# Performance work log

Hardware: AMD Instinct MI355X
Metric: run time of the kernel (lower is better)

Reference implementation:

```python
import jax, jax.numpy as jnp
import numpy as np

B, IN, H, OUT, RANK = 2048, 256, 128, 128, 8
EPS = 1e-5

def setup_inputs() -> dict:
    key = jax.random.key(0)
    ks = jax.random.split(key, 9)
    inv = lambda n: 1.0 / np.sqrt(n)
    return {
        "X": jax.random.normal(ks[0], (B, IN), jnp.float32),
        "W1": jax.random.uniform(ks[1], (IN, H), jnp.float32, -inv(IN), inv(IN)),
        "b1": jnp.zeros((H,), jnp.float32),
        "W2": jax.random.uniform(ks[2], (IN, OUT), jnp.float32, -inv(IN), inv(IN)),
        "b2": jnp.zeros((OUT,), jnp.float32),
        "W3": jax.random.uniform(ks[3], (H, OUT), jnp.float32, -inv(H), inv(H)),
        "b3": jnp.zeros((OUT,), jnp.float32),
        "P": jax.random.normal(ks[4], (RANK, H, H, H), jnp.float32),  # (rank, p, q, k)
        "gz": jnp.ones((H,), jnp.float32),
        "bz": jnp.zeros((H,), jnp.float32),
        "gy": jnp.ones((H,), jnp.float32),
        "by": jnp.zeros((H,), jnp.float32),
    }

def _bn(x, g, b):
    # training-mode BatchNorm1d: batch stats, biased variance
    m = x.mean(axis=0)
    v = x.var(axis=0)
    return (x - m) * jax.lax.rsqrt(v + EPS) * g + b

def reference(X, W1, b1, W2, b2, W3, b3, P, gz, bz, gy, by):
    Z = jax.nn.relu(X @ W1 + b1)               # (B, H); dropout = identity (eval)

    def step(carry, Pi):
        Zi, Y = carry
        # batch_quadratic: out[b,k] = sum_{p,q} Zi[b,p] * Pi[p,q,k] * Z[b,q]
        Zi = jnp.einsum('bp,pqk,bq->bk', Zi, Pi, Z)
        Zi = _bn(Zi, gz, bz)
        return (Zi, Y + Zi / RANK), None

    Y0 = jnp.zeros((X.shape[0], H), X.dtype)
    (_, Y), _ = jax.lax.scan(step, (Z, Y0), P)
    Y = _bn(Y, gy, by)
    out = jax.nn.relu(jax.nn.relu(Y @ W3 + b3) + jax.nn.relu(X @ W2 + b2))
    return out
```

## Files before the change

### kernel.cpp

```cpp
#include <hip/hip_runtime.h>

typedef __bf16 bf16x8 __attribute__((ext_vector_type(8)));
typedef float  floatx4 __attribute__((ext_vector_type(4)));

constexpr int B_    = 2048;
constexpr int NIN   = 256;
constexpr int H_    = 128;
constexpr int RANK_ = 8;
constexpr float EPS_ = 1e-5f;

__global__ __launch_bounds__(256)
void k_head(const float* __restrict__ X,
            const float* __restrict__ W1, const float* __restrict__ b1,
            const float* __restrict__ W2, const float* __restrict__ b2,
            const float* __restrict__ P,
            float* __restrict__ R2, __bf16* __restrict__ Zbf,
            __bf16* __restrict__ Pperm, float* __restrict__ stats ) {
    __shared__ float smem[4160];
    const int bx = blockIdx.x, t = threadIdx.x;

    if (bx < RANK_ + 1) stats[bx * 256 + t] = 0.f;

    if (bx < 512) {
        const int b0 = bx * 4;
#pragma unroll
        for (int i = 0; i < 4; ++i) {
            const int e = i * 256 + t;
            smem[e] = X[(size_t)(b0 + (e >> 8)) * NIN + (e & 255)];
        }
        __syncthreads();
        const int col = t & 127, rh = t >> 7;
        float s1a = 0.f, s2a = 0.f, s1b = 0.f, s2b = 0.f;
        const float* sxa = smem + rh * 256;
        const float* sxb = smem + (rh + 2) * 256;
#pragma unroll 8
        for (int i = 0; i < NIN; ++i) {
            const float w1 = W1[i * H_ + col];
            const float w2 = W2[i * H_ + col];
            s1a = fmaf(sxa[i], w1, s1a);  s2a = fmaf(sxa[i], w2, s2a);
            s1b = fmaf(sxb[i], w1, s1b);  s2b = fmaf(sxb[i], w2, s2b);
        }
        const int ba = b0 + rh, bb = b0 + rh + 2;
        const float za = fmaxf(s1a + b1[col], 0.f), ra = fmaxf(s2a + b2[col], 0.f);
        const float zb = fmaxf(s1b + b1[col], 0.f), rb = fmaxf(s2b + b2[col], 0.f);
        Zbf[(size_t)ba * H_ + col] = (__bf16)za;  R2[(size_t)ba * H_ + col] = ra;
        Zbf[(size_t)bb * H_ + col] = (__bf16)zb;  R2[(size_t)bb * H_ + col] = rb;
        __syncthreads();
    }
    {
        const int r = bx >> 7, p = bx & 127;
        const float4* Pp4 = (const float4*)(P + ((size_t)r * H_ + p) * (H_ * H_));
        __bf16* dst = Pperm + (size_t)r * (H_ * H_ * H_);
        const int L = t & 63, quad = L >> 4, lo = L & 15, g0 = t >> 6;

        float4 rg[4][4];
#pragma unroll
        for (int s = 0; s < 4; ++s)
#pragma unroll
            for (int it = 0; it < 4; ++it) {
                const int idx = it * 256 + t;
                rg[s][it] = Pp4[(size_t)(s * 32 + (idx >> 5)) * 32 + (idx & 31)];
            }
#pragma unroll
        for (int s = 0; s < 4; ++s) {
            if (s) __syncthreads();
#pragma unroll
            for (int it = 0; it < 4; ++it) {
                const int idx = it * 256 + t;
                float* d = smem + (idx >> 5) * 129 + (idx & 31) * 4;
                d[0] = rg[s][it].x; d[1] = rg[s][it].y;
                d[2] = rg[s][it].z; d[3] = rg[s][it].w;
            }
            __syncthreads();
#pragma unroll
            for (int gg = 0; gg < 2; ++gg) {
                const int g = g0 + 4 * gg;
                __bf16 v8[8];
#pragma unroll
                for (int j = 0; j < 8; ++j)
                    v8[j] = (__bf16)smem[(quad * 8 + j) * 129 + g * 16 + lo];
                *(bf16x8*)(dst + (((size_t)(g * 128 + p) * 4 + s) * 64 + L) * 8) =
                    *(const bf16x8*)v8;
            }
        }
    }
}

__global__ __launch_bounds__(512, 2)
void k_rank(const __bf16* __restrict__ Pr, const __bf16* __restrict__ Zbf,
            const float* __restrict__ prevT, const float* __restrict__ prevStats,
            const float* __restrict__ gz, const float* __restrict__ bz,
            float* __restrict__ T, float* __restrict__ stats, const int first) {
    __shared__ float smem[8960];
    const int kg = blockIdx.x, mblk = blockIdx.y, b0 = mblk * 64;
    const int t = threadIdx.x;
    const int w = t >> 6, L = t & 63, quad = L >> 4, lo = L & 15;

    float* sAl = smem + 8704; float* sBe = smem + 8832;
    if (!first && t < 128) {
        const float s1 = prevStats[t], s2 = prevStats[128 + t];
        const float mm = s1 * (1.f / B_);
        const float var = s2 * (1.f / B_) - mm * mm;
        const float a = rsqrtf(var + EPS_) * gz[t];
        sAl[t] = a; sBe[t] = bz[t] - mm * a;
    }
    bf16x8 A[4][4];
#pragma unroll
    for (int mt = 0; mt < 4; ++mt)
#pragma unroll
        for (int ks = 0; ks < 4; ++ks)
            A[mt][ks] = *(const bf16x8*)(Zbf + (size_t)(b0 + mt * 16 + lo) * H_ + ks * 32 + quad * 8);

    const bf16x8* Pb = (const bf16x8*)Pr;
    const int p0 = w * 16;
    const size_t fbase = ((size_t)kg * 128 + p0) * 4;

#define LOADB(dst, pl) do {                                                   \
    _Pragma("unroll") for (int s_ = 0; s_ < 4; ++s_)                          \
        dst[s_] = Pb[(fbase + (size_t)(pl) * 4 + s_) * 64 + L];               \
} while (0)

    bf16x8 B0[4], B1[4], B2[4], B3[4];
    LOADB(B0, 0);
    LOADB(B1, 1);
    LOADB(B2, 2);
    LOADB(B3, 3);

    __syncthreads();
    {
        const int sp = t & 127, rr = t >> 7;
        if (first) {
#pragma unroll
            for (int i = 0; i < 16; ++i) {
                const int row = rr + 4 * i;
                smem[sp * 68 + row] = (float)Zbf[(size_t)(b0 + row) * H_ + sp];
            }
        } else {
            const float a = sAl[sp], be = sBe[sp];
#pragma unroll
            for (int i = 0; i < 16; ++i) {
                const int row = rr + 4 * i;
                smem[sp * 68 + row] = fmaf(prevT[(size_t)(b0 + row) * H_ + sp], a, be);
            }
        }
    }
    __syncthreads();

    floatx4 acc[4];
#pragma unroll
    for (int mt = 0; mt < 4; ++mt) acc[mt] = (floatx4){0.f, 0.f, 0.f, 0.f};

#define COMPUTE(Bx, pg) do {                                                  \
    floatx4 S_[4];                                                            \
    __builtin_amdgcn_s_setprio(1);                                            \
    _Pragma("unroll") for (int mt_ = 0; mt_ < 4; ++mt_)                       \
        S_[mt_] = __builtin_amdgcn_mfma_f32_16x16x32_bf16(                    \
            A[mt_][0], Bx[0], (floatx4){0.f, 0.f, 0.f, 0.f}, 0, 0, 0);        \
    _Pragma("unroll") for (int ks_ = 1; ks_ < 4; ++ks_)                       \
        _Pragma("unroll") for (int mt_ = 0; mt_ < 4; ++mt_)                   \
            S_[mt_] = __builtin_amdgcn_mfma_f32_16x16x32_bf16(                \
                A[mt_][ks_], Bx[ks_], S_[mt_], 0, 0, 0);                      \
    __builtin_amdgcn_s_setprio(0);                                            \
    _Pragma("unroll") for (int mt_ = 0; mt_ < 4; ++mt_) {                     \
        const floatx4 zi_ =                                                   \
            *(const floatx4*)&smem[(pg) * 68 + mt_ * 16 + quad * 4];          \
        acc[mt_] += zi_ * S_[mt_];                                            \
    }                                                                         \
} while (0)

#pragma unroll
    for (int pp = 0; pp < 16; pp += 4) {
        COMPUTE(B0, p0 + pp);     if (pp < 12) LOADB(B0, pp + 4);
        COMPUTE(B1, p0 + pp + 1); if (pp < 12) LOADB(B1, pp + 5);
        COMPUTE(B2, p0 + pp + 2); if (pp < 12) LOADB(B2, pp + 6);
        COMPUTE(B3, p0 + pp + 3); if (pp < 12) LOADB(B3, pp + 7);
    }
#undef LOADB
#undef COMPUTE

    __syncthreads();
#pragma unroll
    for (int mt = 0; mt < 4; ++mt)
#pragma unroll
        for (int i = 0; i < 4; ++i)
            smem[w * 1024 + (mt * 4 + i) * 64 + L] = acc[mt][i];
    if (t < 32) smem[8192 + t] = 0.f;
    __syncthreads();

    float cs = 0.f, cs2 = 0.f;
#pragma unroll
    for (int k2 = 0; k2 < 2; ++k2) {
        const int e = t + 512 * k2;
        float v = 0.f;
#pragma unroll
        for (int q = 0; q < 8; ++q) v += smem[q * 1024 + e];
        const int j = e >> 6, L2 = e & 63;
        const int row = b0 + (j >> 2) * 16 + (L2 >> 4) * 4 + (j & 3);
        const int col = kg * 16 + (L2 & 15);
        T[(size_t)row * H_ + col] = v;
        cs += v; cs2 += v * v;
    }
    cs  += __shfl_xor(cs, 16);  cs  += __shfl_xor(cs, 32);
    cs2 += __shfl_xor(cs2, 16); cs2 += __shfl_xor(cs2, 32);
    if (L < 16) { atomicAdd(&smem[8192 + L], cs); atomicAdd(&smem[8208 + L], cs2); }
    __syncthreads();
    if (t < 16)      atomicAdd(&stats[kg * 16 + t],            smem[8192 + t]);
    else if (t < 32) atomicAdd(&stats[128 + kg * 16 + t - 16], smem[8192 + t]);
}

__global__ __launch_bounds__(256)
void k_y(const float* __restrict__ T, const float* __restrict__ sums,
         const float* __restrict__ gz, const float* __restrict__ bz,
         float* __restrict__ Y, float* __restrict__ ysums) {
    __shared__ float al[1024], be[1024], red[256];
    const int bx = blockIdx.x, t = threadIdx.x;
    for (int e = t; e < 1024; e += 256) {
        const int rr = e >> 7, k = e & 127;
        const float s1 = sums[rr * 256 + k], s2 = sums[rr * 256 + 128 + k];
        const float mm = s1 * (1.f / B_);
        const float var = s2 * (1.f / B_) - mm * mm;
        const float a = rsqrtf(var + EPS_) * gz[k];
        al[e] = a; be[e] = bz[k] - mm * a;
    }
    red[t] = 0.f;
    __syncthreads();
    const int col = t & 127, half = t >> 7;
    float ps = 0.f, ps2 = 0.f;
    for (int i = 0; i < 16; ++i) {
        const int b = bx * 32 + half + 2 * i;
        float y = 0.f;
#pragma unroll
        for (int rr = 0; rr < 8; ++rr)
            y += fmaf(T[(size_t)rr * B_ * H_ + (size_t)b * H_ + col],
                      al[rr * 128 + col], be[rr * 128 + col]);
        y *= (1.f / RANK_);
        Y[(size_t)b * H_ + col] = y;
        ps += y; ps2 += y * y;
    }
    atomicAdd(&red[col],       half == 0 ? ps  : 0.f);
    atomicAdd(&red[128 + col], half == 0 ? ps2 : 0.f);
    __syncthreads();
    atomicAdd(&red[col],       half == 1 ? ps  : 0.f);
    atomicAdd(&red[128 + col], half == 1 ? ps2 : 0.f);
    __syncthreads();
    if (t < 128) {
        atomicAdd(&ysums[t],       red[t]);
        atomicAdd(&ysums[128 + t], red[128 + t]);
    }
}

__global__ __launch_bounds__(256)
void k_out(const float* __restrict__ Y, const float* __restrict__ ystats,
           const float* __restrict__ gy, const float* __restrict__ by,
           const float* __restrict__ W3, const float* __restrict__ b3,
           const float* __restrict__ R2, float* __restrict__ out) {
    __shared__ float sy[8 * 132];
    const int bx = blockIdx.x, t = threadIdx.x;
    const int col = t & 127, rh = t >> 7;
    const int b0 = bx * 8;
    const float mm = ystats[col] * (1.f / B_);
    const float var = ystats[128 + col] * (1.f / B_) - mm * mm;
    const float ay = rsqrtf(var + EPS_) * gy[col];
    const float bb = by[col] - mm * ay;
#pragma unroll
    for (int i = 0; i < 4; ++i) {
        const int row = rh + 2 * i;
        sy[row * 132 + col] = fmaf(Y[(size_t)(b0 + row) * H_ + col], ay, bb);
    }
    __syncthreads();
#pragma unroll
    for (int j = 0; j < 4; ++j) {
        const int row = rh * 4 + j;
        float s = 0.f;
        const float* syr = sy + row * 132;
#pragma unroll 8
        for (int h = 0; h < H_; ++h)
            s = fmaf(syr[h], W3[h * H_ + col], s);
        const size_t gi = (size_t)(b0 + row) * H_ + col;
        out[gi] = fmaxf(fmaxf(s + b3[col], 0.f) + R2[gi], 0.f);
    }
}

extern "C" void kernel_launch(void* const* d_in, const int* in_sizes, int n_in,
                              void* d_out, int out_size, void* d_ws, size_t ws_size,
                              hipStream_t stream) {
    const float* X  = (const float*)d_in[0];
    const float* W1 = (const float*)d_in[1];
    const float* b1 = (const float*)d_in[2];
    const float* W2 = (const float*)d_in[3];
    const float* b2 = (const float*)d_in[4];
    const float* W3 = (const float*)d_in[5];
    const float* b3 = (const float*)d_in[6];
    const float* P  = (const float*)d_in[7];
    const float* gz = (const float*)d_in[8];
    const float* bz = (const float*)d_in[9];
    const float* gy = (const float*)d_in[10];
    const float* by = (const float*)d_in[11];
    float* out = (float*)d_out;

    const size_t rankElems = (size_t)H_ * H_ * H_;

    char* wsb = (char*)d_ws;
    float* R2     = (float*)wsb;   wsb += (size_t)B_ * H_ * 4;
    float* Y      = (float*)wsb;   wsb += (size_t)B_ * H_ * 4;
    float* stats  = (float*)wsb;   wsb += (size_t)(RANK_ + 1) * 256 * 4;
    float* T      = (float*)wsb;   wsb += (size_t)RANK_ * B_ * H_ * 4;
    __bf16* Zbf   = (__bf16*)wsb;  wsb += (size_t)B_ * H_ * 2;
    __bf16* Pperm = (__bf16*)wsb;

    float* ysums = stats + RANK_ * 256;

    k_head<<<1024, 256, 0, stream>>>(X, W1, b1, W2, b2, P, R2, Zbf, Pperm, stats);

    for (int r = 0; r < RANK_; ++r) {
        const float* prevT = (r == 0) ? (const float*)Zbf : (T + (size_t)(r - 1) * B_ * H_);
        const float* prevS = (r == 0) ? stats : (stats + (r - 1) * 256);
        k_rank<<<dim3(8, 32), 512, 0, stream>>>(Pperm + (size_t)r * rankElems, Zbf,
                                                prevT, prevS, gz, bz,
                                                T + (size_t)r * B_ * H_, stats + r * 256,
                                                r == 0 ? 1 : 0);
    }

    k_y<<<64, 256, 0, stream>>>(T, stats, gz, bz, Y, ysums);
    k_out<<<256, 256, 0, stream>>>(Y, ysums, gy, by, W3, b3, R2, out);
}
```

Before: 275.2 us.

## Halve batch tile in rank kernel and head GEMM to raise block count

The rank kernel now handles 32 batch rows per block instead of 64, launching 512 blocks instead of 256, with half the A fragments, accumulators, shared memory and a two-deep instead of four-deep B prefetch, and launch bounds raised to allow 4 blocks per CU. The head kernel computes 2 rows per block across all 1024 blocks instead of 4 rows in the first 512. The aim is better occupancy and CU coverage on the small grid. The cost is that each block re-reads the full P slice for half as many rows, doubling P traffic per rank step, and the shallower prefetch hides less load latency.

```diff
diff --git a/kernel.cpp b/kernel.cpp
--- a/kernel.cpp
+++ b/kernel.cpp
@@ -21,30 +21,26 @@
 
     if (bx < RANK_ + 1) stats[bx * 256 + t] = 0.f;
 
-    if (bx < 512) {
-        const int b0 = bx * 4;
-#pragma unroll
-        for (int i = 0; i < 4; ++i) {
+    {
+        const int b0 = bx * 2;
+#pragma unroll
+        for (int i = 0; i < 2; ++i) {
             const int e = i * 256 + t;
             smem[e] = X[(size_t)(b0 + (e >> 8)) * NIN + (e & 255)];
         }
         __syncthreads();
         const int col = t & 127, rh = t >> 7;
-        float s1a = 0.f, s2a = 0.f, s1b = 0.f, s2b = 0.f;
-        const float* sxa = smem + rh * 256;
-        const float* sxb = smem + (rh + 2) * 256;
-#pragma unroll 8
+        float s1 = 0.f, s2 = 0.f;
+        const float* sx = smem + rh * 256;
+#pragma unroll 16
         for (int i = 0; i < NIN; ++i) {
             const float w1 = W1[i * H_ + col];
             const float w2 = W2[i * H_ + col];
-            s1a = fmaf(sxa[i], w1, s1a);  s2a = fmaf(sxa[i], w2, s2a);
-            s1b = fmaf(sxb[i], w1, s1b);  s2b = fmaf(sxb[i], w2, s2b);
+            s1 = fmaf(sx[i], w1, s1);  s2 = fmaf(sx[i], w2, s2);
         }
-        const int ba = b0 + rh, bb = b0 + rh + 2;
-        const float za = fmaxf(s1a + b1[col], 0.f), ra = fmaxf(s2a + b2[col], 0.f);
-        const float zb = fmaxf(s1b + b1[col], 0.f), rb = fmaxf(s2b + b2[col], 0.f);
-        Zbf[(size_t)ba * H_ + col] = (__bf16)za;  R2[(size_t)ba * H_ + col] = ra;
-        Zbf[(size_t)bb * H_ + col] = (__bf16)zb;  R2[(size_t)bb * H_ + col] = rb;
+        const int br = b0 + rh;
+        const float z = fmaxf(s1 + b1[col], 0.f), r = fmaxf(s2 + b2[col], 0.f);
+        Zbf[(size_t)br * H_ + col] = (__bf16)z;  R2[(size_t)br * H_ + col] = r;
         __syncthreads();
     }
     {
@@ -86,17 +82,17 @@
     }
 }
 
-__global__ __launch_bounds__(512, 2)
+__global__ __launch_bounds__(512, 4)
 void k_rank(const __bf16* __restrict__ Pr, const __bf16* __restrict__ Zbf,
             const float* __restrict__ prevT, const float* __restrict__ prevStats,
             const float* __restrict__ gz, const float* __restrict__ bz,
             float* __restrict__ T, float* __restrict__ stats, const int first) {
-    __shared__ float smem[8960];
-    const int kg = blockIdx.x, mblk = blockIdx.y, b0 = mblk * 64;
+    __shared__ float smem[4864];
+    const int kg = blockIdx.x, mblk = blockIdx.y, b0 = mblk * 32;
     const int t = threadIdx.x;
     const int w = t >> 6, L = t & 63, quad = L >> 4, lo = L & 15;
 
-    float* sAl = smem + 8704; float* sBe = smem + 8832;
+    float* sAl = smem + 4608; float* sBe = smem + 4736;
     if (!first && t < 128) {
         const float s1 = prevStats[t], s2 = prevStats[128 + t];
         const float mm = s1 * (1.f / B_);
@@ -104,9 +100,9 @@
         const float a = rsqrtf(var + EPS_) * gz[t];
         sAl[t] = a; sBe[t] = bz[t] - mm * a;
     }
-    bf16x8 A[4][4];
-#pragma unroll
-    for (int mt = 0; mt < 4; ++mt)
+    bf16x8 A[2][4];
+#pragma unroll
+    for (int mt = 0; mt < 2; ++mt)
 #pragma unroll
         for (int ks = 0; ks < 4; ++ks)
             A[mt][ks] = *(const bf16x8*)(Zbf + (size_t)(b0 + mt * 16 + lo) * H_ + ks * 32 + quad * 8);
@@ -120,92 +116,83 @@
         dst[s_] = Pb[(fbase + (size_t)(pl) * 4 + s_) * 64 + L];               \
 } while (0)
 
-    bf16x8 B0[4], B1[4], B2[4], B3[4];
+    bf16x8 B0[4], B1[4];
     LOADB(B0, 0);
     LOADB(B1, 1);
-    LOADB(B2, 2);
-    LOADB(B3, 3);
 
     __syncthreads();
     {
         const int sp = t & 127, rr = t >> 7;
         if (first) {
 #pragma unroll
-            for (int i = 0; i < 16; ++i) {
+            for (int i = 0; i < 8; ++i) {
                 const int row = rr + 4 * i;
-                smem[sp * 68 + row] = (float)Zbf[(size_t)(b0 + row) * H_ + sp];
+                smem[sp * 36 + row] = (float)Zbf[(size_t)(b0 + row) * H_ + sp];
             }
         } else {
             const float a = sAl[sp], be = sBe[sp];
 #pragma unroll
-            for (int i = 0; i < 16; ++i) {
+            for (int i = 0; i < 8; ++i) {
                 const int row = rr + 4 * i;
-                smem[sp * 68 + row] = fmaf(prevT[(size_t)(b0 + row) * H_ + sp], a, be);
+                smem[sp * 36 + row] = fmaf(prevT[(size_t)(b0 + row) * H_ + sp], a, be);
             }
         }
     }
     __syncthreads();
 
-    floatx4 acc[4];
-#pragma unroll
-    for (int mt = 0; mt < 4; ++mt) acc[mt] = (floatx4){0.f, 0.f, 0.f, 0.f};
+    floatx4 acc[2];
+#pragma unroll
+    for (int mt = 0; mt < 2; ++mt) acc[mt] = (floatx4){0.f, 0.f, 0.f, 0.f};
 
 #define COMPUTE(Bx, pg) do {                                                  \
-    floatx4 S_[4];                                                            \
+    floatx4 S_[2];                                                            \
     __builtin_amdgcn_s_setprio(1);                                            \
-    _Pragma("unroll") for (int mt_ = 0; mt_ < 4; ++mt_)                       \
+    _Pragma("unroll") for (int mt_ = 0; mt_ < 2; ++mt_)                       \
         S_[mt_] = __builtin_amdgcn_mfma_f32_16x16x32_bf16(                    \
             A[mt_][0], Bx[0], (floatx4){0.f, 0.f, 0.f, 0.f}, 0, 0, 0);        \
     _Pragma("unroll") for (int ks_ = 1; ks_ < 4; ++ks_)                       \
-        _Pragma("unroll") for (int mt_ = 0; mt_ < 4; ++mt_)                   \
+        _Pragma("unroll") for (int mt_ = 0; mt_ < 2; ++mt_)                   \
             S_[mt_] = __builtin_amdgcn_mfma_f32_16x16x32_bf16(                \
                 A[mt_][ks_], Bx[ks_], S_[mt_], 0, 0, 0);                      \
     __builtin_amdgcn_s_setprio(0);                                            \
-    _Pragma("unroll") for (int mt_ = 0; mt_ < 4; ++mt_) {                     \
+    _Pragma("unroll") for (int mt_ = 0; mt_ < 2; ++mt_) {                     \
         const floatx4 zi_ =                                                   \
-            *(const floatx4*)&smem[(pg) * 68 + mt_ * 16 + quad * 4];          \
+            *(const floatx4*)&smem[(pg) * 36 + mt_ * 16 + quad * 4];          \
         acc[mt_] += zi_ * S_[mt_];                                            \
     }                                                                         \
 } while (0)
 
 #pragma unroll
-    for (int pp = 0; pp < 16; pp += 4) {
-        COMPUTE(B0, p0 + pp);     if (pp < 12) LOADB(B0, pp + 4);
-        COMPUTE(B1, p0 + pp + 1); if (pp < 12) LOADB(B1, pp + 5);
-        COMPUTE(B2, p0 + pp + 2); if (pp < 12) LOADB(B2, pp + 6);
-        COMPUTE(B3, p0 + pp + 3); if (pp < 12) LOADB(B3, pp + 7);
+    for (int pp = 0; pp < 16; pp += 2) {
+        COMPUTE(B0, p0 + pp);     if (pp < 14) LOADB(B0, pp + 2);
+        COMPUTE(B1, p0 + pp + 1); if (pp < 14) LOADB(B1, pp + 3);
     }
 #undef LOADB
 #undef COMPUTE
 
     __syncthreads();
 #pragma unroll
-    for (int mt = 0; mt < 4; ++mt)
+    for (int mt = 0; mt < 2; ++mt)
 #pragma unroll
         for (int i = 0; i < 4; ++i)
-            smem[w * 1024 + (mt * 4 + i) * 64 + L] = acc[mt][i];
-    if (t < 32) smem[8192 + t] = 0.f;
-    __syncthreads();
-
-    float cs = 0.f, cs2 = 0.f;
-#pragma unroll
-    for (int k2 = 0; k2 < 2; ++k2) {
-        const int e = t + 512 * k2;
-        float v = 0.f;
-#pragma unroll
-        for (int q = 0; q < 8; ++q) v += smem[q * 1024 + e];
-        const int j = e >> 6, L2 = e & 63;
-        const int row = b0 + (j >> 2) * 16 + (L2 >> 4) * 4 + (j & 3);
-        const int col = kg * 16 + (L2 & 15);
-        T[(size_t)row * H_ + col] = v;
-        cs += v; cs2 += v * v;
-    }
+            smem[w * 512 + (mt * 4 + i) * 64 + L] = acc[mt][i];
+    if (t < 32) smem[4096 + t] = 0.f;
+    __syncthreads();
+
+    float v = 0.f;
+#pragma unroll
+    for (int q = 0; q < 8; ++q) v += smem[q * 512 + t];
+    const int j = t >> 6, L2 = t & 63;
+    const int row = b0 + (j >> 2) * 16 + (L2 >> 4) * 4 + (j & 3);
+    const int col = kg * 16 + (L2 & 15);
+    T[(size_t)row * H_ + col] = v;
+    float cs = v, cs2 = v * v;
     cs  += __shfl_xor(cs, 16);  cs  += __shfl_xor(cs, 32);
     cs2 += __shfl_xor(cs2, 16); cs2 += __shfl_xor(cs2, 32);
-    if (L < 16) { atomicAdd(&smem[8192 + L], cs); atomicAdd(&smem[8208 + L], cs2); }
-    __syncthreads();
-    if (t < 16)      atomicAdd(&stats[kg * 16 + t],            smem[8192 + t]);
-    else if (t < 32) atomicAdd(&stats[128 + kg * 16 + t - 16], smem[8192 + t]);
+    if (L < 16) { atomicAdd(&smem[4096 + L], cs); atomicAdd(&smem[4112 + L], cs2); }
+    __syncthreads();
+    if (t < 16)      atomicAdd(&stats[kg * 16 + t],            smem[4096 + t]);
+    else if (t < 32) atomicAdd(&stats[128 + kg * 16 + t - 16], smem[4096 + t]);
 }
 
 __global__ __launch_bounds__(256)
@@ -315,7 +302,7 @@
     for (int r = 0; r < RANK_; ++r) {
         const float* prevT = (r == 0) ? (const float*)Zbf : (T + (size_t)(r - 1) * B_ * H_);
         const float* prevS = (r == 0) ? stats : (stats + (r - 1) * 256);
-        k_rank<<<dim3(8, 32), 512, 0, stream>>>(Pperm + (size_t)r * rankElems, Zbf,
+        k_rank<<<dim3(8, 64), 512, 0, stream>>>(Pperm + (size_t)r * rankElems, Zbf,
                                                 prevT, prevS, gz, bz,
                                                 T + (size_t)r * B_ * H_, stats + r * 256,
                                                 r == 0 ? 1 : 0);
```

After: 283.9 us. +3.1%, slower.

## Fuse per-rank launches into one cooperative kernel with grid sync

Applied to the files above, without the earlier changes.

Replaces the eight separate k_rank launches with a single cooperative k_ranks kernel that loops over ranks and uses grid.sync between them, removing per-launch overhead and ramp-up/tail gaps. The head kernel also now spreads the X@W1/X@W2 work across all 1024 blocks (2 rows each) instead of 512 blocks with 4 rows. Cooperative launch needs all 256 blocks to be co-resident and adds grid-barrier cost. The head change trades per-thread reuse of weight loads for better balance.

```diff
diff --git a/kernel.cpp b/kernel.cpp
--- a/kernel.cpp
+++ b/kernel.cpp
@@ -1,4 +1,7 @@
 #include <hip/hip_runtime.h>
+#include <hip/hip_cooperative_groups.h>
+
+namespace cg = cooperative_groups;
 
 typedef __bf16 bf16x8 __attribute__((ext_vector_type(8)));
 typedef float  floatx4 __attribute__((ext_vector_type(4)));
@@ -21,30 +24,26 @@
 
     if (bx < RANK_ + 1) stats[bx * 256 + t] = 0.f;
 
-    if (bx < 512) {
-        const int b0 = bx * 4;
-#pragma unroll
-        for (int i = 0; i < 4; ++i) {
+    {
+        const int b0 = bx * 2;
+#pragma unroll
+        for (int i = 0; i < 2; ++i) {
             const int e = i * 256 + t;
             smem[e] = X[(size_t)(b0 + (e >> 8)) * NIN + (e & 255)];
         }
         __syncthreads();
         const int col = t & 127, rh = t >> 7;
-        float s1a = 0.f, s2a = 0.f, s1b = 0.f, s2b = 0.f;
-        const float* sxa = smem + rh * 256;
-        const float* sxb = smem + (rh + 2) * 256;
-#pragma unroll 8
+        float s1 = 0.f, s2 = 0.f;
+        const float* sx = smem + rh * 256;
+#pragma unroll 16
         for (int i = 0; i < NIN; ++i) {
             const float w1 = W1[i * H_ + col];
             const float w2 = W2[i * H_ + col];
-            s1a = fmaf(sxa[i], w1, s1a);  s2a = fmaf(sxa[i], w2, s2a);
-            s1b = fmaf(sxb[i], w1, s1b);  s2b = fmaf(sxb[i], w2, s2b);
-        }
-        const int ba = b0 + rh, bb = b0 + rh + 2;
-        const float za = fmaxf(s1a + b1[col], 0.f), ra = fmaxf(s2a + b2[col], 0.f);
-        const float zb = fmaxf(s1b + b1[col], 0.f), rb = fmaxf(s2b + b2[col], 0.f);
-        Zbf[(size_t)ba * H_ + col] = (__bf16)za;  R2[(size_t)ba * H_ + col] = ra;
-        Zbf[(size_t)bb * H_ + col] = (__bf16)zb;  R2[(size_t)bb * H_ + col] = rb;
+            s1 = fmaf(sx[i], w1, s1);  s2 = fmaf(sx[i], w2, s2);
+        }
+        const int br = b0 + rh;
+        const float z = fmaxf(s1 + b1[col], 0.f), r = fmaxf(s2 + b2[col], 0.f);
+        Zbf[(size_t)br * H_ + col] = (__bf16)z;  R2[(size_t)br * H_ + col] = r;
         __syncthreads();
     }
     {
@@ -87,23 +86,15 @@
 }
 
 __global__ __launch_bounds__(512, 2)
-void k_rank(const __bf16* __restrict__ Pr, const __bf16* __restrict__ Zbf,
-            const float* __restrict__ prevT, const float* __restrict__ prevStats,
-            const float* __restrict__ gz, const float* __restrict__ bz,
-            float* __restrict__ T, float* __restrict__ stats, const int first) {
+void k_ranks(const __bf16* __restrict__ Pperm, const __bf16* __restrict__ Zbf,
+             const float* __restrict__ gz, const float* __restrict__ bz,
+             float* __restrict__ T, float* __restrict__ stats) {
     __shared__ float smem[8960];
     const int kg = blockIdx.x, mblk = blockIdx.y, b0 = mblk * 64;
     const int t = threadIdx.x;
     const int w = t >> 6, L = t & 63, quad = L >> 4, lo = L & 15;
-
     float* sAl = smem + 8704; float* sBe = smem + 8832;
-    if (!first && t < 128) {
-        const float s1 = prevStats[t], s2 = prevStats[128 + t];
-        const float mm = s1 * (1.f / B_);
-        const float var = s2 * (1.f / B_) - mm * mm;
-        const float a = rsqrtf(var + EPS_) * gz[t];
-        sAl[t] = a; sBe[t] = bz[t] - mm * a;
-    }
+
     bf16x8 A[4][4];
 #pragma unroll
     for (int mt = 0; mt < 4; ++mt)
@@ -111,44 +102,57 @@
         for (int ks = 0; ks < 4; ++ks)
             A[mt][ks] = *(const bf16x8*)(Zbf + (size_t)(b0 + mt * 16 + lo) * H_ + ks * 32 + quad * 8);
 
-    const bf16x8* Pb = (const bf16x8*)Pr;
     const int p0 = w * 16;
     const size_t fbase = ((size_t)kg * 128 + p0) * 4;
+    cg::grid_group grid = cg::this_grid();
+
+    for (int r = 0; r < RANK_; ++r) {
+        const bf16x8* Pb = (const bf16x8*)(Pperm + (size_t)r * (H_ * H_ * H_));
+        const float* prevT = T + (size_t)(r - 1) * B_ * H_;
+        float* Tr = T + (size_t)r * B_ * H_;
+        float* statsr = stats + r * 256;
 
 #define LOADB(dst, pl) do {                                                   \
     _Pragma("unroll") for (int s_ = 0; s_ < 4; ++s_)                          \
         dst[s_] = Pb[(fbase + (size_t)(pl) * 4 + s_) * 64 + L];               \
 } while (0)
 
-    bf16x8 B0[4], B1[4], B2[4], B3[4];
-    LOADB(B0, 0);
-    LOADB(B1, 1);
-    LOADB(B2, 2);
-    LOADB(B3, 3);
-
-    __syncthreads();
-    {
-        const int sp = t & 127, rr = t >> 7;
-        if (first) {
-#pragma unroll
-            for (int i = 0; i < 16; ++i) {
-                const int row = rr + 4 * i;
-                smem[sp * 68 + row] = (float)Zbf[(size_t)(b0 + row) * H_ + sp];
+        bf16x8 B0[4], B1[4], B2[4], B3[4];
+        LOADB(B0, 0);
+        LOADB(B1, 1);
+        LOADB(B2, 2);
+        LOADB(B3, 3);
+
+        if (r && t < 128) {
+            const float s1 = stats[(r - 1) * 256 + t], s2 = stats[(r - 1) * 256 + 128 + t];
+            const float mm = s1 * (1.f / B_);
+            const float var = s2 * (1.f / B_) - mm * mm;
+            const float a = rsqrtf(var + EPS_) * gz[t];
+            sAl[t] = a; sBe[t] = bz[t] - mm * a;
+        }
+        __syncthreads();
+        {
+            const int sp = t & 127, rr = t >> 7;
+            if (r == 0) {
+#pragma unroll
+                for (int i = 0; i < 16; ++i) {
+                    const int row = rr + 4 * i;
+                    smem[sp * 68 + row] = (float)Zbf[(size_t)(b0 + row) * H_ + sp];
+                }
+            } else {
+                const float a = sAl[sp], be = sBe[sp];
+#pragma unroll
+                for (int i = 0; i < 16; ++i) {
+                    const int row = rr + 4 * i;
+                    smem[sp * 68 + row] = fmaf(prevT[(size_t)(b0 + row) * H_ + sp], a, be);
+                }
             }
-        } else {
-            const float a = sAl[sp], be = sBe[sp];
-#pragma unroll
-            for (int i = 0; i < 16; ++i) {
-                const int row = rr + 4 * i;
-                smem[sp * 68 + row] = fmaf(prevT[(size_t)(b0 + row) * H_ + sp], a, be);
-            }
-        }
-    }
-    __syncthreads();
-
-    floatx4 acc[4];
-#pragma unroll
-    for (int mt = 0; mt < 4; ++mt) acc[mt] = (floatx4){0.f, 0.f, 0.f, 0.f};
+        }
+        __syncthreads();
+
+        floatx4 acc[4];
+#pragma unroll
+        for (int mt = 0; mt < 4; ++mt) acc[mt] = (floatx4){0.f, 0.f, 0.f, 0.f};
 
 #define COMPUTE(Bx, pg) do {                                                  \
     floatx4 S_[4];                                                            \
@@ -169,43 +173,49 @@
 } while (0)
 
 #pragma unroll
-    for (int pp = 0; pp < 16; pp += 4) {
-        COMPUTE(B0, p0 + pp);     if (pp < 12) LOADB(B0, pp + 4);
-        COMPUTE(B1, p0 + pp + 1); if (pp < 12) LOADB(B1, pp + 5);
-        COMPUTE(B2, p0 + pp + 2); if (pp < 12) LOADB(B2, pp + 6);
-        COMPUTE(B3, p0 + pp + 3); if (pp < 12) LOADB(B3, pp + 7);
-    }
+        for (int pp = 0; pp < 16; pp += 4) {
+            COMPUTE(B0, p0 + pp);     if (pp < 12) LOADB(B0, pp + 4);
+            COMPUTE(B1, p0 + pp + 1); if (pp < 12) LOADB(B1, pp + 5);
+            COMPUTE(B2, p0 + pp + 2); if (pp < 12) LOADB(B2, pp + 6);
+            COMPUTE(B3, p0 + pp + 3); if (pp < 12) LOADB(B3, pp + 7);
+        }
 #undef LOADB
 #undef COMPUTE
 
-    __syncthreads();
-#pragma unroll
-    for (int mt = 0; mt < 4; ++mt)
-#pragma unroll
-        for (int i = 0; i < 4; ++i)
-            smem[w * 1024 + (mt * 4 + i) * 64 + L] = acc[mt][i];
-    if (t < 32) smem[8192 + t] = 0.f;
-    __syncthreads();
-
-    float cs = 0.f, cs2 = 0.f;
-#pragma unroll
-    for (int k2 = 0; k2 < 2; ++k2) {
-        const int e = t + 512 * k2;
-        float v = 0.f;
-#pragma unroll
-        for (int q = 0; q < 8; ++q) v += smem[q * 1024 + e];
-        const int j = e >> 6, L2 = e & 63;
-        const int row = b0 + (j >> 2) * 16 + (L2 >> 4) * 4 + (j & 3);
-        const int col = kg * 16 + (L2 & 15);
-        T[(size_t)row * H_ + col] = v;
-        cs += v; cs2 += v * v;
-    }
-    cs  += __shfl_xor(cs, 16);  cs  += __shfl_xor(cs, 32);
-    cs2 += __shfl_xor(cs2, 16); cs2 += __shfl_xor(cs2, 32);
-    if (L < 16) { atomicAdd(&smem[8192 + L], cs); atomicAdd(&smem[8208 + L], cs2); }
-    __syncthreads();
-    if (t < 16)      atomicAdd(&stats[kg * 16 + t],            smem[8192 + t]);
-    else if (t < 32) atomicAdd(&stats[128 + kg * 16 + t - 16], smem[8192 + t]);
+        __syncthreads();
+#pragma unroll
+        for (int mt = 0; mt < 4; ++mt)
+#pragma unroll
+            for (int i = 0; i < 4; ++i)
+                smem[w * 1024 + (mt * 4 + i) * 64 + L] = acc[mt][i];
+        if (t < 32) smem[8192 + t] = 0.f;
+        __syncthreads();
+
+        float cs = 0.f, cs2 = 0.f;
+#pragma unroll
+        for (int k2 = 0; k2 < 2; ++k2) {
+            const int e = t + 512 * k2;
+            float v = 0.f;
+#pragma unroll
+            for (int q = 0; q < 8; ++q) v += smem[q * 1024 + e];
+            const int j = e >> 6, L2 = e & 63;
+            const int row = b0 + (j >> 2) * 16 + (L2 >> 4) * 4 + (j & 3);
+            const int col = kg * 16 + (L2 & 15);
+            Tr[(size_t)row * H_ + col] = v;
+            cs += v; cs2 += v * v;
+        }
+        cs  += __shfl_xor(cs, 16);  cs  += __shfl_xor(cs, 32);
+        cs2 += __shfl_xor(cs2, 16); cs2 += __shfl_xor(cs2, 32);
+        if (L < 16) { atomicAdd(&smem[8192 + L], cs); atomicAdd(&smem[8208 + L], cs2); }
+        __syncthreads();
+        if (t < 16)      atomicAdd(&statsr[kg * 16 + t],            smem[8192 + t]);
+        else if (t < 32) atomicAdd(&statsr[128 + kg * 16 + t - 16], smem[8192 + t]);
+
+        if (r < RANK_ - 1) {
+            __threadfence();
+            grid.sync();
+        }
+    }
 }
 
 __global__ __launch_bounds__(256)
@@ -298,8 +308,6 @@
     const float* by = (const float*)d_in[11];
     float* out = (float*)d_out;
 
-    const size_t rankElems = (size_t)H_ * H_ * H_;
-
     char* wsb = (char*)d_ws;
     float* R2     = (float*)wsb;   wsb += (size_t)B_ * H_ * 4;
     float* Y      = (float*)wsb;   wsb += (size_t)B_ * H_ * 4;
@@ -312,13 +320,17 @@
 
     k_head<<<1024, 256, 0, stream>>>(X, W1, b1, W2, b2, P, R2, Zbf, Pperm, stats);
 
-    for (int r = 0; r < RANK_; ++r) {
-        const float* prevT = (r == 0) ? (const float*)Zbf : (T + (size_t)(r - 1) * B_ * H_);
-        const float* prevS = (r == 0) ? stats : (stats + (r - 1) * 256);
-        k_rank<<<dim3(8, 32), 512, 0, stream>>>(Pperm + (size_t)r * rankElems, Zbf,
-                                                prevT, prevS, gz, bz,
-                                                T + (size_t)r * B_ * H_, stats + r * 256,
-                                                r == 0 ? 1 : 0);
+    {
+        const __bf16* Pperm_c = Pperm;
+        const __bf16* Zbf_c   = Zbf;
+        const float*  gz_c    = gz;
+        const float*  bz_c    = bz;
+        float*        T_c     = T;
+        float*        stats_c = stats;
+        void* kargs[6] = { (void*)&Pperm_c, (void*)&Zbf_c, (void*)&gz_c,
+                           (void*)&bz_c, (void*)&T_c, (void*)&stats_c };
+        hipLaunchCooperativeKernel((void*)k_ranks, dim3(8, 32), dim3(512),
+                                   kargs, 0, stream);
     }
 
     k_y<<<64, 256, 0, stream>>>(T, stats, gz, bz, Y, ysums);
```

Result: slower. 721.9 us (+162.3%).

## Replace global stat atomics with per-block partials and vectorize prev-T staging

Applied to the files above, without the earlier changes.

Each k_rank block now writes its per-column sum and sum-of-squares partials to a dedicated slot instead of doing global atomicAdds. The consumer (the next rank kernel or k_y) reduces the 32 partials itself, and the BN-coefficient computation moves after the B prefetch loads. The prev-T/Z staging into shared memory now uses float4/ushort4 loads. k_head also spreads the X@W1/W2 work over all 1024 blocks with one row per thread, instead of 512 blocks with two rows each. The changes remove atomic contention and cross-block nondeterminism, in exchange for extra partial-buffer reads in every consumer.

```diff
diff --git a/kernel.cpp b/kernel.cpp
--- a/kernel.cpp
+++ b/kernel.cpp
@@ -21,30 +21,26 @@
 
     if (bx < RANK_ + 1) stats[bx * 256 + t] = 0.f;
 
-    if (bx < 512) {
-        const int b0 = bx * 4;
-#pragma unroll
-        for (int i = 0; i < 4; ++i) {
+    {
+        const int b0 = bx * 2;
+#pragma unroll
+        for (int i = 0; i < 2; ++i) {
             const int e = i * 256 + t;
             smem[e] = X[(size_t)(b0 + (e >> 8)) * NIN + (e & 255)];
         }
         __syncthreads();
         const int col = t & 127, rh = t >> 7;
-        float s1a = 0.f, s2a = 0.f, s1b = 0.f, s2b = 0.f;
-        const float* sxa = smem + rh * 256;
-        const float* sxb = smem + (rh + 2) * 256;
-#pragma unroll 8
+        float s1 = 0.f, s2 = 0.f;
+        const float* sx = smem + rh * 256;
+#pragma unroll 16
         for (int i = 0; i < NIN; ++i) {
             const float w1 = W1[i * H_ + col];
             const float w2 = W2[i * H_ + col];
-            s1a = fmaf(sxa[i], w1, s1a);  s2a = fmaf(sxa[i], w2, s2a);
-            s1b = fmaf(sxb[i], w1, s1b);  s2b = fmaf(sxb[i], w2, s2b);
-        }
-        const int ba = b0 + rh, bb = b0 + rh + 2;
-        const float za = fmaxf(s1a + b1[col], 0.f), ra = fmaxf(s2a + b2[col], 0.f);
-        const float zb = fmaxf(s1b + b1[col], 0.f), rb = fmaxf(s2b + b2[col], 0.f);
-        Zbf[(size_t)ba * H_ + col] = (__bf16)za;  R2[(size_t)ba * H_ + col] = ra;
-        Zbf[(size_t)bb * H_ + col] = (__bf16)zb;  R2[(size_t)bb * H_ + col] = rb;
+            s1 = fmaf(sx[i], w1, s1);  s2 = fmaf(sx[i], w2, s2);
+        }
+        const int br = b0 + rh;
+        const float z = fmaxf(s1 + b1[col], 0.f), r = fmaxf(s2 + b2[col], 0.f);
+        Zbf[(size_t)br * H_ + col] = (__bf16)z;  R2[(size_t)br * H_ + col] = r;
         __syncthreads();
     }
     {
@@ -88,22 +84,15 @@
 
 __global__ __launch_bounds__(512, 2)
 void k_rank(const __bf16* __restrict__ Pr, const __bf16* __restrict__ Zbf,
-            const float* __restrict__ prevT, const float* __restrict__ prevStats,
+            const float* __restrict__ prevT, const float* __restrict__ prevPart,
             const float* __restrict__ gz, const float* __restrict__ bz,
-            float* __restrict__ T, float* __restrict__ stats, const int first) {
+            float* __restrict__ T, float* __restrict__ ownPart, const int first) {
     __shared__ float smem[8960];
     const int kg = blockIdx.x, mblk = blockIdx.y, b0 = mblk * 64;
     const int t = threadIdx.x;
     const int w = t >> 6, L = t & 63, quad = L >> 4, lo = L & 15;
 
     float* sAl = smem + 8704; float* sBe = smem + 8832;
-    if (!first && t < 128) {
-        const float s1 = prevStats[t], s2 = prevStats[128 + t];
-        const float mm = s1 * (1.f / B_);
-        const float var = s2 * (1.f / B_) - mm * mm;
-        const float a = rsqrtf(var + EPS_) * gz[t];
-        sAl[t] = a; sBe[t] = bz[t] - mm * a;
-    }
     bf16x8 A[4][4];
 #pragma unroll
     for (int mt = 0; mt < 4; ++mt)
@@ -126,21 +115,42 @@
     LOADB(B2, 2);
     LOADB(B3, 3);
 
+    if (!first && t < 128) {
+        float s1 = 0.f, s2 = 0.f;
+#pragma unroll 8
+        for (int m = 0; m < 32; ++m) {
+            s1 += prevPart[m * 128 + t];
+            s2 += prevPart[(32 + m) * 128 + t];
+        }
+        const float mm = s1 * (1.f / B_);
+        const float var = s2 * (1.f / B_) - mm * mm;
+        const float a = rsqrtf(var + EPS_) * gz[t];
+        sAl[t] = a; sBe[t] = bz[t] - mm * a;
+    }
     __syncthreads();
     {
-        const int sp = t & 127, rr = t >> 7;
+        const int cg = t >> 4, rs = t & 15;
         if (first) {
 #pragma unroll
-            for (int i = 0; i < 16; ++i) {
-                const int row = rr + 4 * i;
-                smem[sp * 68 + row] = (float)Zbf[(size_t)(b0 + row) * H_ + sp];
+            for (int i = 0; i < 4; ++i) {
+                const int row = rs + 16 * i;
+                const ushort4 u = *(const ushort4*)(Zbf + (size_t)(b0 + row) * H_ + cg * 4);
+                smem[(cg * 4 + 0) * 68 + row] = __uint_as_float((unsigned)u.x << 16);
+                smem[(cg * 4 + 1) * 68 + row] = __uint_as_float((unsigned)u.y << 16);
+                smem[(cg * 4 + 2) * 68 + row] = __uint_as_float((unsigned)u.z << 16);
+                smem[(cg * 4 + 3) * 68 + row] = __uint_as_float((unsigned)u.w << 16);
             }
         } else {
-            const float a = sAl[sp], be = sBe[sp];
-#pragma unroll
-            for (int i = 0; i < 16; ++i) {
-                const int row = rr + 4 * i;
-                smem[sp * 68 + row] = fmaf(prevT[(size_t)(b0 + row) * H_ + sp], a, be);
+            const float4 al4 = *(const float4*)&sAl[cg * 4];
+            const float4 be4 = *(const float4*)&sBe[cg * 4];
+#pragma unroll
+            for (int i = 0; i < 4; ++i) {
+                const int row = rs + 16 * i;
+                const float4 v = *(const float4*)(prevT + (size_t)(b0 + row) * H_ + cg * 4);
+                smem[(cg * 4 + 0) * 68 + row] = fmaf(v.x, al4.x, be4.x);
+                smem[(cg * 4 + 1) * 68 + row] = fmaf(v.y, al4.y, be4.y);
+                smem[(cg * 4 + 2) * 68 + row] = fmaf(v.z, al4.z, be4.z);
+                smem[(cg * 4 + 3) * 68 + row] = fmaf(v.w, al4.w, be4.w);
             }
         }
     }
@@ -204,19 +214,25 @@
     cs2 += __shfl_xor(cs2, 16); cs2 += __shfl_xor(cs2, 32);
     if (L < 16) { atomicAdd(&smem[8192 + L], cs); atomicAdd(&smem[8208 + L], cs2); }
     __syncthreads();
-    if (t < 16)      atomicAdd(&stats[kg * 16 + t],            smem[8192 + t]);
-    else if (t < 32) atomicAdd(&stats[128 + kg * 16 + t - 16], smem[8192 + t]);
+    if (t < 16)      ownPart[(size_t)mblk * 128 + kg * 16 + t]        = smem[8192 + t];
+    else if (t < 32) ownPart[(size_t)(32 + mblk) * 128 + kg * 16 + t - 16] = smem[8192 + t];
 }
 
 __global__ __launch_bounds__(256)
-void k_y(const float* __restrict__ T, const float* __restrict__ sums,
+void k_y(const float* __restrict__ T, const float* __restrict__ partials,
          const float* __restrict__ gz, const float* __restrict__ bz,
          float* __restrict__ Y, float* __restrict__ ysums) {
     __shared__ float al[1024], be[1024], red[256];
     const int bx = blockIdx.x, t = threadIdx.x;
     for (int e = t; e < 1024; e += 256) {
         const int rr = e >> 7, k = e & 127;
-        const float s1 = sums[rr * 256 + k], s2 = sums[rr * 256 + 128 + k];
+        const float* bp = partials + (size_t)rr * 8192;
+        float s1 = 0.f, s2 = 0.f;
+#pragma unroll 8
+        for (int m = 0; m < 32; ++m) {
+            s1 += bp[m * 128 + k];
+            s2 += bp[(32 + m) * 128 + k];
+        }
         const float mm = s1 * (1.f / B_);
         const float var = s2 * (1.f / B_) - mm * mm;
         const float a = rsqrtf(var + EPS_) * gz[k];
@@ -301,12 +317,13 @@
     const size_t rankElems = (size_t)H_ * H_ * H_;
 
     char* wsb = (char*)d_ws;
-    float* R2     = (float*)wsb;   wsb += (size_t)B_ * H_ * 4;
-    float* Y      = (float*)wsb;   wsb += (size_t)B_ * H_ * 4;
-    float* stats  = (float*)wsb;   wsb += (size_t)(RANK_ + 1) * 256 * 4;
-    float* T      = (float*)wsb;   wsb += (size_t)RANK_ * B_ * H_ * 4;
-    __bf16* Zbf   = (__bf16*)wsb;  wsb += (size_t)B_ * H_ * 2;
-    __bf16* Pperm = (__bf16*)wsb;
+    float* R2       = (float*)wsb;   wsb += (size_t)B_ * H_ * 4;
+    float* Y        = (float*)wsb;   wsb += (size_t)B_ * H_ * 4;
+    float* stats    = (float*)wsb;   wsb += (size_t)(RANK_ + 1) * 256 * 4;
+    float* partials = (float*)wsb;   wsb += (size_t)RANK_ * 2 * 32 * 128 * 4;
+    float* T        = (float*)wsb;   wsb += (size_t)RANK_ * B_ * H_ * 4;
+    __bf16* Zbf     = (__bf16*)wsb;  wsb += (size_t)B_ * H_ * 2;
+    __bf16* Pperm   = (__bf16*)wsb;
 
     float* ysums = stats + RANK_ * 256;
 
@@ -314,13 +331,14 @@
 
     for (int r = 0; r < RANK_; ++r) {
         const float* prevT = (r == 0) ? (const float*)Zbf : (T + (size_t)(r - 1) * B_ * H_);
-        const float* prevS = (r == 0) ? stats : (stats + (r - 1) * 256);
+        const float* prevP = (r == 0) ? partials : (partials + (size_t)(r - 1) * 8192);
         k_rank<<<dim3(8, 32), 512, 0, stream>>>(Pperm + (size_t)r * rankElems, Zbf,
-                                                prevT, prevS, gz, bz,
-                                                T + (size_t)r * B_ * H_, stats + r * 256,
+                                                prevT, prevP, gz, bz,
+                                                T + (size_t)r * B_ * H_,
+                                                partials + (size_t)r * 8192,
                                                 r == 0 ? 1 : 0);
     }
 
-    k_y<<<64, 256, 0, stream>>>(T, stats, gz, bz, Y, ysums);
+    k_y<<<64, 256, 0, stream>>>(T, partials, gz, bz, Y, ysums);
     k_out<<<256, 256, 0, stream>>>(Y, ysums, gy, by, W3, b3, R2, out);
 }
```

Result: slower. 285.5 us (+3.8%).
